# Optimization experiments

Hardware: AMD Instinct MI355X
Metric: run time of the kernel (lower is better)

Reference implementation:

```python
import jax, jax.numpy as jnp
import numpy as np

N_NODES = 50000
N_EDGES = 1600000
IN_CH, HID_CH, OUT_CH = 384, 128, 64


def gcn_conv(x, W, b, src, dst, num_nodes):
    """PyG GCNConv: add self-loops, symmetric deg^-1/2 normalization,
    linear transform, scatter-add aggregation, bias."""
    loop = jnp.arange(num_nodes, dtype=src.dtype)
    src2 = jnp.concatenate([src, loop])  # [E+N]
    dst2 = jnp.concatenate([dst, loop])
    deg = jax.ops.segment_sum(jnp.ones_like(dst2, dtype=x.dtype), dst2,
                              num_segments=num_nodes)
    dinv = jnp.where(deg > 0, jax.lax.rsqrt(deg), 0.0)
    norm = dinv[src2] * dinv[dst2]  # [E+N]
    h = x @ W  # [N, out]
    msg = h[src2] * norm[:, None]  # gather + scale
    out = jax.ops.segment_sum(msg, dst2, num_segments=num_nodes)
    return out + b


def setup_inputs() -> dict:
    key = jax.random.key(0)
    k1, k2, k3, k4 = jax.random.split(key, 4)
    x = jax.random.normal(k1, (N_NODES, IN_CH), dtype=jnp.float32)
    edge_index = jax.random.randint(k2, (2, N_EDGES), 0, N_NODES, dtype=jnp.int64)
    W1 = jax.random.normal(k3, (IN_CH, HID_CH), dtype=jnp.float32) / np.sqrt(IN_CH)
    b1 = jnp.zeros((HID_CH,), dtype=jnp.float32)
    W2 = jax.random.normal(k4, (HID_CH, OUT_CH), dtype=jnp.float32) / np.sqrt(HID_CH)
    b2 = jnp.zeros((OUT_CH,), dtype=jnp.float32)
    return {"x": x, "edge_index": edge_index, "W1": W1, "b1": b1, "W2": W2, "b2": b2}


def reference(x, edge_index, W1, b1, W2, b2):
    src, dst = edge_index[0], edge_index[1]
    h = gcn_conv(x, W1, b1, src, dst, N_NODES)
    h = jax.nn.relu(h)
    out = gcn_conv(h, W2, b2, src, dst, N_NODES)
    return out
```

## Files before the change

kernel.cpp:

```cpp
#include <hip/hip_runtime.h>

constexpr int NN  = 50000;
constexpr int NE  = 1600000;
constexpr int CIN = 384;
constexpr int CH  = 128;
constexpr int CO  = 64;

constexpr int NB = (NN + 255) / 256;
constexpr int BUCKET_CAP = 16384;
constexpr int SCAT_EPB     = 4096;
constexpr int SCAT_BLOCKS  = (NE + SCAT_EPB - 1) / SCAT_EPB;
constexpr int G1_TILES     = (NN + 127) / 128;
constexpr int G2_TILES     = (NN + 127) / 128;

typedef __attribute__((ext_vector_type(8))) short short8;
typedef __attribute__((ext_vector_type(4))) float f32x4;


__device__ inline unsigned short f2bf(float f) {
    union { float f; unsigned int u; } v; v.f = f;
    unsigned int u = v.u + 0x7FFFu + ((v.u >> 16) & 1u);
    return (unsigned short)(u >> 16);
}
__device__ inline float bf2f(unsigned short h) { return __uint_as_float((unsigned int)h << 16); }
__device__ inline float bflo(unsigned int u) { return __uint_as_float(u << 16); }
__device__ inline float bfhi(unsigned int u) { return __uint_as_float(u & 0xFFFF0000u); }


__global__ __launch_bounds__(256) void wprep(const float* __restrict__ W1, const float* __restrict__ W2,
                                             unsigned short* __restrict__ W1t_hi, unsigned short* __restrict__ W1t_lo,
                                             unsigned short* __restrict__ W2t_hi, unsigned short* __restrict__ W2t_lo,
                                             int* __restrict__ bucket_cursor) {
    int i = blockIdx.x * 256 + threadIdx.x;
    if (blockIdx.x == 0 && threadIdx.x < NB)
        bucket_cursor[threadIdx.x] = threadIdx.x * BUCKET_CAP;
    if (i < CIN * CH) {
        int k = i / CH, c = i % CH;
        float v = W1[i];
        unsigned short h = f2bf(v);
        W1t_hi[c * CIN + k] = h;
        W1t_lo[c * CIN + k] = f2bf(v - bf2f(h));
    } else if (i < CIN * CH + CH * CO) {
        int j = i - CIN * CH;
        int k = j / CO, c = j % CO;
        float v = W2[j];
        unsigned short h = f2bf(v);
        W2t_hi[c * CH + k] = h;
        W2t_lo[c * CH + k] = f2bf(v - bf2f(h));
    }
}


__global__ __launch_bounds__(256) void fused_gemm1_scatter(const int* __restrict__ src,
                                                           const int* __restrict__ dst,
                                                           int* __restrict__ bucket_cursor,
                                                           unsigned int* __restrict__ pairs,
                                                           const float* __restrict__ X,
                                                           const unsigned short* __restrict__ Wt_hi,
                                                           const unsigned short* __restrict__ Wt_lo,
                                                           unsigned short* __restrict__ Hb) {
    __shared__ unsigned short xs_hi[128][40];
    __shared__ unsigned short xs_lo[128][40];
    __shared__ unsigned short ws_hi[128][40];
    __shared__ unsigned short ws_lo[128][40];
    __shared__ int hist[NB];
    __shared__ int base_s[NB];

    int tid = threadIdx.x;
    if (blockIdx.x < SCAT_BLOCKS) {
        int e0 = blockIdx.x * SCAT_EPB;
        for (int i = tid; i < NB; i += 256) hist[i] = 0;
        __syncthreads();
        int key[16];
        unsigned int pay[16];
        #pragma unroll
        for (int k = 0; k < 16; ++k) {
            int e = e0 + k * 256 + tid;
            if (e < NE) {
                int s = src[e], d = dst[e];
                int b = d >> 8;
                int pos = atomicAdd(&hist[b], 1);
                key[k] = b | (pos << 8);
                pay[k] = (unsigned int)s | ((unsigned int)(d & 255) << 16);
            } else {
                key[k] = -1;
            }
        }
        __syncthreads();
        for (int i = tid; i < NB; i += 256)
            base_s[i] = hist[i] ? atomicAdd(&bucket_cursor[i], hist[i]) : 0;
        __syncthreads();
        #pragma unroll
        for (int k = 0; k < 16; ++k) {
            if (key[k] >= 0) {
                int b = key[k] & 255, pos = key[k] >> 8;
                pairs[base_s[b] + pos] = pay[k];
            }
        }
        return;
    }

    int wid = tid >> 6, lane = tid & 63;
    int row0 = (blockIdx.x - SCAT_BLOCKS) * 128;
    f32x4 acc[2][8] = {};

    int xrow = tid >> 1, xc = (tid & 1) * 16;
    int grow = row0 + xrow;
    int wcol = tid >> 2, wko = (tid & 3) * 8;

    float xf[16];
    short8 pwh0, pwl0, pwh1, pwl1;

    auto loadX = [&](int k0) {
        if (grow < NN) {
            const float4* p = reinterpret_cast<const float4*>(X + (size_t)grow * CIN + k0 + xc);
            float4 v0 = p[0], v1 = p[1], v2 = p[2], v3 = p[3];
            xf[0]=v0.x; xf[1]=v0.y; xf[2]=v0.z; xf[3]=v0.w;
            xf[4]=v1.x; xf[5]=v1.y; xf[6]=v1.z; xf[7]=v1.w;
            xf[8]=v2.x; xf[9]=v2.y; xf[10]=v2.z; xf[11]=v2.w;
            xf[12]=v3.x; xf[13]=v3.y; xf[14]=v3.z; xf[15]=v3.w;
        } else {
            #pragma unroll
            for (int i = 0; i < 16; ++i) xf[i] = 0.f;
        }
    };
    auto loadW = [&](int k0) {
        pwh0 = *reinterpret_cast<const short8*>(Wt_hi + (size_t)wcol * CIN + k0 + wko);
        pwl0 = *reinterpret_cast<const short8*>(Wt_lo + (size_t)wcol * CIN + k0 + wko);
        pwh1 = *reinterpret_cast<const short8*>(Wt_hi + (size_t)(wcol + 64) * CIN + k0 + wko);
        pwl1 = *reinterpret_cast<const short8*>(Wt_lo + (size_t)(wcol + 64) * CIN + k0 + wko);
    };

    loadX(0); loadW(0);
    for (int k0 = 0; k0 < CIN; k0 += 32) {
        {
            short8 vh0, vh1, vl0, vl1;
            #pragma unroll
            for (int i = 0; i < 8; ++i) {
                unsigned short h = f2bf(xf[i]);
                vh0[i] = (short)h; vl0[i] = (short)f2bf(xf[i] - bf2f(h));
            }
            #pragma unroll
            for (int i = 0; i < 8; ++i) {
                unsigned short h = f2bf(xf[8 + i]);
                vh1[i] = (short)h; vl1[i] = (short)f2bf(xf[8 + i] - bf2f(h));
            }
            *reinterpret_cast<short8*>(&xs_hi[xrow][xc])     = vh0;
            *reinterpret_cast<short8*>(&xs_hi[xrow][xc + 8]) = vh1;
            *reinterpret_cast<short8*>(&xs_lo[xrow][xc])     = vl0;
            *reinterpret_cast<short8*>(&xs_lo[xrow][xc + 8]) = vl1;
            *reinterpret_cast<short8*>(&ws_hi[wcol][wko])      = pwh0;
            *reinterpret_cast<short8*>(&ws_lo[wcol][wko])      = pwl0;
            *reinterpret_cast<short8*>(&ws_hi[wcol + 64][wko]) = pwh1;
            *reinterpret_cast<short8*>(&ws_lo[wcol + 64][wko]) = pwl1;
        }
        __syncthreads();
        if (k0 + 32 < CIN) { loadX(k0 + 32); loadW(k0 + 32); }
        int r = lane & 15, ko = (lane >> 4) * 8;
        short8 a_hi[2], a_lo[2];
        #pragma unroll
        for (int rt = 0; rt < 2; ++rt) {
            a_hi[rt] = *reinterpret_cast<const short8*>(&xs_hi[wid * 32 + rt * 16 + r][ko]);
            a_lo[rt] = *reinterpret_cast<const short8*>(&xs_lo[wid * 32 + rt * 16 + r][ko]);
        }
        #pragma unroll
        for (int ct = 0; ct < 8; ++ct) {
            short8 b_hi = *reinterpret_cast<const short8*>(&ws_hi[ct * 16 + r][ko]);
            short8 b_lo = *reinterpret_cast<const short8*>(&ws_lo[ct * 16 + r][ko]);
            #pragma unroll
            for (int rt = 0; rt < 2; ++rt) {
                acc[rt][ct] = __builtin_amdgcn_mfma_f32_16x16x32_bf16(a_hi[rt], b_hi, acc[rt][ct], 0, 0, 0);
                acc[rt][ct] = __builtin_amdgcn_mfma_f32_16x16x32_bf16(a_hi[rt], b_lo, acc[rt][ct], 0, 0, 0);
                acc[rt][ct] = __builtin_amdgcn_mfma_f32_16x16x32_bf16(a_lo[rt], b_hi, acc[rt][ct], 0, 0, 0);
            }
        }
        __syncthreads();
    }
    int cl = lane & 15, rg = lane >> 4;
    #pragma unroll
    for (int rt = 0; rt < 2; ++rt) {
        #pragma unroll
        for (int j = 0; j < 4; ++j) {
            int row = row0 + wid * 32 + rt * 16 + rg * 4 + j;
            if (row < NN) {
                unsigned short* hp = Hb + (size_t)row * CH + cl;
                #pragma unroll
                for (int ct = 0; ct < 8; ++ct)
                    hp[ct * 16] = f2bf(acc[rt][ct][j]);
            }
        }
    }
}


__global__ __launch_bounds__(256) void bucket_scan(const int* __restrict__ bucket_cursor,
                                                   int* __restrict__ bucket_start) {
    __shared__ int tmp[256];
    int t = threadIdx.x;
    int v = (t < NB) ? (bucket_cursor[t] - t * BUCKET_CAP) : 0;
    tmp[t] = v;
    __syncthreads();
    for (int off = 1; off < 256; off <<= 1) {
        int add = (t >= off) ? tmp[t - off] : 0;
        __syncthreads();
        tmp[t] += add;
        __syncthreads();
    }
    if (t < NB) bucket_start[t] = tmp[t] - v;
    if (t == NB - 1) bucket_start[NB] = tmp[t];
}


__global__ __launch_bounds__(1024) void bucket_sort(const unsigned int* __restrict__ pairs,
                                                    const int* __restrict__ bucket_cursor,
                                                    const int* __restrict__ bucket_start,
                                                    int* __restrict__ row_start,
                                                    float* __restrict__ dinv,
                                                    unsigned short* __restrict__ csr_src) {
    __shared__ int cnt[256];
    __shared__ int pref[256];
    __shared__ int cur[256];
    int b = blockIdx.x, t = threadIdx.x;
    int p0 = b * BUCKET_CAP;
    int ne = bucket_cursor[b] - p0;
    int out0 = bucket_start[b];
    if (t < 256) cnt[t] = 0;
    __syncthreads();
    for (int i = t; i < ne; i += 1024)
        atomicAdd(&cnt[(pairs[p0 + i] >> 16) & 255], 1);
    __syncthreads();
    if (t < 256) pref[t] = cnt[t];
    __syncthreads();
    for (int off = 1; off < 256; off <<= 1) {
        int add = (t < 256 && t >= off) ? pref[t - off] : 0;
        __syncthreads();
        if (t < 256) pref[t] += add;
        __syncthreads();
    }
    if (t < 256) {
        int n = (b << 8) + t;
        if (n < NN) {
            int rs = out0 + pref[t] - cnt[t];
            row_start[n] = rs;
            cur[t] = rs;
            dinv[n] = rsqrtf((float)(cnt[t] + 1));
        }
    }
    if (b == NB - 1 && t == 0) row_start[NN] = NE;
    __syncthreads();
    for (int i = t; i < ne; i += 1024) {
        unsigned int p = pairs[p0 + i];
        int pos = atomicAdd(&cur[(p >> 16) & 255], 1);
        csr_src[pos] = (unsigned short)(p & 0xFFFF);
    }
}


__global__ __launch_bounds__(256) void gemm2_kernel(const float* __restrict__ X,
                                                    const unsigned short* __restrict__ Wt_hi,
                                                    const unsigned short* __restrict__ Wt_lo,
                                                    unsigned short* __restrict__ Hb) {
    __shared__ unsigned short xs_hi[128][40];
    __shared__ unsigned short xs_lo[128][40];
    __shared__ unsigned short ws_hi[64][40];
    __shared__ unsigned short ws_lo[64][40];

    int tid = threadIdx.x;
    int wid = tid >> 6, lane = tid & 63;
    int row0 = blockIdx.x * 128;
    f32x4 acc[2][4] = {};

    for (int k0 = 0; k0 < CH; k0 += 32) {
        {
            int row = tid >> 1, c = (tid & 1) * 16;
            int grow = row0 + row;
            float f[16];
            if (grow < NN) {
                const float4* p = reinterpret_cast<const float4*>(X + (size_t)grow * CH + k0 + c);
                float4 v0 = p[0], v1 = p[1], v2 = p[2], v3 = p[3];
                f[0]=v0.x; f[1]=v0.y; f[2]=v0.z; f[3]=v0.w;
                f[4]=v1.x; f[5]=v1.y; f[6]=v1.z; f[7]=v1.w;
                f[8]=v2.x; f[9]=v2.y; f[10]=v2.z; f[11]=v2.w;
                f[12]=v3.x; f[13]=v3.y; f[14]=v3.z; f[15]=v3.w;
            } else {
                #pragma unroll
                for (int i = 0; i < 16; ++i) f[i] = 0.f;
            }
            short8 vh0, vh1, vl0, vl1;
            #pragma unroll
            for (int i = 0; i < 8; ++i) {
                unsigned short h = f2bf(f[i]);
                vh0[i] = (short)h; vl0[i] = (short)f2bf(f[i] - bf2f(h));
            }
            #pragma unroll
            for (int i = 0; i < 8; ++i) {
                unsigned short h = f2bf(f[8 + i]);
                vh1[i] = (short)h; vl1[i] = (short)f2bf(f[8 + i] - bf2f(h));
            }
            *reinterpret_cast<short8*>(&xs_hi[row][c])     = vh0;
            *reinterpret_cast<short8*>(&xs_hi[row][c + 8]) = vh1;
            *reinterpret_cast<short8*>(&xs_lo[row][c])     = vl0;
            *reinterpret_cast<short8*>(&xs_lo[row][c + 8]) = vl1;
        }
        if (tid < 256) {
            int col = tid >> 2, ko = (tid & 3) * 8;
            *reinterpret_cast<short8*>(&ws_hi[col][ko]) =
                *reinterpret_cast<const short8*>(Wt_hi + (size_t)col * CH + k0 + ko);
            *reinterpret_cast<short8*>(&ws_lo[col][ko]) =
                *reinterpret_cast<const short8*>(Wt_lo + (size_t)col * CH + k0 + ko);
        }
        __syncthreads();
        int r = lane & 15, ko = (lane >> 4) * 8;
        short8 a_hi[2], a_lo[2];
        #pragma unroll
        for (int rt = 0; rt < 2; ++rt) {
            a_hi[rt] = *reinterpret_cast<const short8*>(&xs_hi[wid * 32 + rt * 16 + r][ko]);
            a_lo[rt] = *reinterpret_cast<const short8*>(&xs_lo[wid * 32 + rt * 16 + r][ko]);
        }
        #pragma unroll
        for (int ct = 0; ct < 4; ++ct) {
            short8 b_hi = *reinterpret_cast<const short8*>(&ws_hi[ct * 16 + r][ko]);
            short8 b_lo = *reinterpret_cast<const short8*>(&ws_lo[ct * 16 + r][ko]);
            #pragma unroll
            for (int rt = 0; rt < 2; ++rt) {
                acc[rt][ct] = __builtin_amdgcn_mfma_f32_16x16x32_bf16(a_hi[rt], b_hi, acc[rt][ct], 0, 0, 0);
                acc[rt][ct] = __builtin_amdgcn_mfma_f32_16x16x32_bf16(a_hi[rt], b_lo, acc[rt][ct], 0, 0, 0);
                acc[rt][ct] = __builtin_amdgcn_mfma_f32_16x16x32_bf16(a_lo[rt], b_hi, acc[rt][ct], 0, 0, 0);
            }
        }
        __syncthreads();
    }
    int cl = lane & 15, rg = lane >> 4;
    #pragma unroll
    for (int rt = 0; rt < 2; ++rt) {
        #pragma unroll
        for (int j = 0; j < 4; ++j) {
            int row = row0 + wid * 32 + rt * 16 + rg * 4 + j;
            if (row < NN) {
                unsigned short* hp = Hb + (size_t)row * CO + cl;
                #pragma unroll
                for (int ct = 0; ct < 4; ++ct)
                    hp[ct * 16] = f2bf(acc[rt][ct][j]);
            }
        }
    }
}


__global__ __launch_bounds__(64) void agg1_kernel(const unsigned int* __restrict__ H,
                                                  const int* __restrict__ row_start,
                                                  const unsigned short* __restrict__ csr_src,
                                                  const float* __restrict__ dinv,
                                                  const float* __restrict__ bias,
                                                  float* __restrict__ OUT) {
    int n = blockIdx.x;
    int l = threadIdx.x;
    float dn = dinv[n];
    unsigned int us = H[n * 64 + l];
    float a0 = dn * bflo(us), a1 = dn * bfhi(us);
    float b0 = 0.f, b1 = 0.f, c0 = 0.f, c1 = 0.f, d0 = 0.f, d1 = 0.f;
    float e0a = 0.f, e1a = 0.f, f0 = 0.f, f1 = 0.f, g0 = 0.f, g1v = 0.f, h0 = 0.f, h1 = 0.f;
    int e0 = row_start[n], e1 = row_start[n + 1];
    for (int base = e0; base < e1; base += 64) {
        int m = min(64, e1 - base);
        int sv = csr_src[base + min(l, m - 1)];
        float wv = (l < m) ? dinv[sv] : 0.f;
        int j = 0;
        for (; j + 8 <= m; j += 8) {
            int s0 = __shfl(sv, j),     s1 = __shfl(sv, j + 1);
            int s2 = __shfl(sv, j + 2), s3 = __shfl(sv, j + 3);
            int s4 = __shfl(sv, j + 4), s5 = __shfl(sv, j + 5);
            int s6 = __shfl(sv, j + 6), s7 = __shfl(sv, j + 7);
            float w0 = __shfl(wv, j),     w1 = __shfl(wv, j + 1);
            float w2 = __shfl(wv, j + 2), w3 = __shfl(wv, j + 3);
            float w4 = __shfl(wv, j + 4), w5 = __shfl(wv, j + 5);
            float w6 = __shfl(wv, j + 6), w7 = __shfl(wv, j + 7);
            unsigned int u0 = H[s0 * 64 + l];
            unsigned int u1 = H[s1 * 64 + l];
            unsigned int u2 = H[s2 * 64 + l];
            unsigned int u3 = H[s3 * 64 + l];
            unsigned int u4 = H[s4 * 64 + l];
            unsigned int u5 = H[s5 * 64 + l];
            unsigned int u6 = H[s6 * 64 + l];
            unsigned int u7 = H[s7 * 64 + l];
            a0  = fmaf(w0, bflo(u0), a0);  a1  = fmaf(w0, bfhi(u0), a1);
            b0  = fmaf(w1, bflo(u1), b0);  b1  = fmaf(w1, bfhi(u1), b1);
            c0  = fmaf(w2, bflo(u2), c0);  c1  = fmaf(w2, bfhi(u2), c1);
            d0  = fmaf(w3, bflo(u3), d0);  d1  = fmaf(w3, bfhi(u3), d1);
            e0a = fmaf(w4, bflo(u4), e0a); e1a = fmaf(w4, bfhi(u4), e1a);
            f0  = fmaf(w5, bflo(u5), f0);  f1  = fmaf(w5, bfhi(u5), f1);
            g0  = fmaf(w6, bflo(u6), g0);  g1v = fmaf(w6, bfhi(u6), g1v);
            h0  = fmaf(w7, bflo(u7), h0);  h1  = fmaf(w7, bfhi(u7), h1);
        }
        for (; j < m; ++j) {
            int s0 = __shfl(sv, j);
            float w0 = __shfl(wv, j);
            unsigned int u0 = H[s0 * 64 + l];
            a0 = fmaf(w0, bflo(u0), a0); a1 = fmaf(w0, bfhi(u0), a1);
        }
    }
    float s0 = ((a0 + b0) + (c0 + d0)) + ((e0a + f0) + (g0 + h0));
    float s1 = ((a1 + b1) + (c1 + d1)) + ((e1a + f1) + (g1v + h1));
    float2 bv = reinterpret_cast<const float2*>(bias)[l];
    float o0 = fmaf(dn, s0, bv.x);
    float o1 = fmaf(dn, s1, bv.y);
    reinterpret_cast<float2*>(OUT)[n * 64 + l] = make_float2(fmaxf(o0, 0.f), fmaxf(o1, 0.f));
}

__global__ __launch_bounds__(64) void agg2_kernel(const unsigned int* __restrict__ H,
                                                  const int* __restrict__ row_start,
                                                  const unsigned short* __restrict__ csr_src,
                                                  const float* __restrict__ dinv,
                                                  const float* __restrict__ bias,
                                                  float* __restrict__ OUT) {
    int n = blockIdx.x;
    int l = threadIdx.x;
    int half = l >> 5;
    int c = l & 31;
    float dn = dinv[n];
    unsigned int us = H[n * 32 + c];
    float a0 = half ? 0.f : dn * bflo(us);
    float a1 = half ? 0.f : dn * bfhi(us);
    float b0 = 0.f, b1 = 0.f, c0 = 0.f, c1 = 0.f, d0 = 0.f, d1 = 0.f;
    int e0 = row_start[n], e1 = row_start[n + 1];
    for (int base = e0; base < e1; base += 64) {
        int m = min(64, e1 - base);
        int sv = csr_src[base + min(l, m - 1)];
        float wv = (l < m) ? dinv[sv] : 0.f;
        int j = 0;
        for (; j + 8 <= m; j += 8) {
            int jj0 = j + half, jj1 = j + 2 + half, jj2 = j + 4 + half, jj3 = j + 6 + half;
            int s0 = __shfl(sv, jj0), s1 = __shfl(sv, jj1);
            int s2 = __shfl(sv, jj2), s3 = __shfl(sv, jj3);
            float w0 = __shfl(wv, jj0), w1 = __shfl(wv, jj1);
            float w2 = __shfl(wv, jj2), w3 = __shfl(wv, jj3);
            unsigned int u0 = H[s0 * 32 + c];
            unsigned int u1 = H[s1 * 32 + c];
            unsigned int u2 = H[s2 * 32 + c];
            unsigned int u3 = H[s3 * 32 + c];
            a0 = fmaf(w0, bflo(u0), a0); a1 = fmaf(w0, bfhi(u0), a1);
            b0 = fmaf(w1, bflo(u1), b0); b1 = fmaf(w1, bfhi(u1), b1);
            c0 = fmaf(w2, bflo(u2), c0); c1 = fmaf(w2, bfhi(u2), c1);
            d0 = fmaf(w3, bflo(u3), d0); d1 = fmaf(w3, bfhi(u3), d1);
        }
        for (; j < m; j += 2) {
            int jj = j + half;
            int s = __shfl(sv, min(jj, m - 1));
            float w = __shfl(wv, jj);
            unsigned int u = H[s * 32 + c];
            a0 = fmaf(w, bflo(u), a0);
            a1 = fmaf(w, bfhi(u), a1);
        }
    }
    a0 = (a0 + b0) + (c0 + d0);
    a1 = (a1 + b1) + (c1 + d1);
    a0 += __shfl_xor(a0, 32);
    a1 += __shfl_xor(a1, 32);
    if (l < 32) {
        float2 bv = reinterpret_cast<const float2*>(bias)[c];
        float o0 = fmaf(dn, a0, bv.x);
        float o1 = fmaf(dn, a1, bv.y);
        reinterpret_cast<float2*>(OUT)[n * 32 + c] = make_float2(o0, o1);
    }
}


extern "C" void kernel_launch(void* const* d_in, const int* in_sizes, int n_in,
                              void* d_out, int out_size, void* d_ws, size_t ws_size,
                              hipStream_t stream) {
    const float* x  = (const float*)d_in[0];
    const int*   ei = (const int*)d_in[1];
    const float* W1 = (const float*)d_in[2];
    const float* b1 = (const float*)d_in[3];
    const float* W2 = (const float*)d_in[4];
    const float* b2 = (const float*)d_in[5];
    const int* srcI = ei;
    const int* dstI = ei + NE;
    float* out = (float*)d_out;

    char* ws = (char*)d_ws;
    size_t off = 0;
    auto take = [&](size_t bytes) {
        char* p = ws + off;
        off = (off + bytes + 255) & ~(size_t)255;
        return p;
    };
    int*            row_start     = (int*)take((size_t)(NN + 1) * 4);
    int*            bucket_cursor = (int*)take((size_t)NB * 4);
    int*            bucket_start  = (int*)take((size_t)(NB + 1) * 4);
    float*          dinv          = (float*)take((size_t)NN * 4);
    unsigned short* W1t_hi        = (unsigned short*)take((size_t)CH * CIN * 2);
    unsigned short* W1t_lo        = (unsigned short*)take((size_t)CH * CIN * 2);
    unsigned short* W2t_hi        = (unsigned short*)take((size_t)CO * CH * 2);
    unsigned short* W2t_lo        = (unsigned short*)take((size_t)CO * CH * 2);
    unsigned short* csr_src       = (unsigned short*)take((size_t)NE * 2);
    unsigned short* h1b           = (unsigned short*)take((size_t)NN * CH * 2);
    float*          g1            = (float*)take((size_t)NN * CH * 4);
    unsigned short* h2b           = (unsigned short*)take((size_t)NN * CO * 2);
    unsigned int*   pairs         = (unsigned int*)g1;

    wprep<<<(CIN * CH + CH * CO + 255) / 256, 256, 0, stream>>>(W1, W2, W1t_hi, W1t_lo,
                                                                W2t_hi, W2t_lo, bucket_cursor);
    fused_gemm1_scatter<<<SCAT_BLOCKS + G1_TILES, 256, 0, stream>>>(srcI, dstI, bucket_cursor,
                                                                    pairs, x, W1t_hi, W1t_lo, h1b);
    bucket_scan<<<1, 256, 0, stream>>>(bucket_cursor, bucket_start);
    bucket_sort<<<NB, 1024, 0, stream>>>(pairs, bucket_cursor, bucket_start,
                                         row_start, dinv, csr_src);

    agg1_kernel<<<NN, 64, 0, stream>>>((const unsigned int*)h1b, row_start, csr_src, dinv, b1, g1);
    gemm2_kernel<<<G2_TILES, 256, 0, stream>>>(g1, W2t_hi, W2t_lo, h2b);
    agg2_kernel<<<NN, 64, 0, stream>>>((const unsigned int*)h2b, row_start, csr_src, dinv, b2, out);
}
```

Measured before the change: 153.1 us.

## Fuse layer-2 GEMM into layer-1 aggregation and interleave scatter/GEMM1 blocks

The separate gemm2 MFMA kernel is removed. Each agg1 block now applies ReLU, then multiplies its 128-wide node row by W2 with a wavefront-shuffle GEMV in fp32, writing bf16 H2 directly. This avoids writing and rereading the fp32 g1 intermediate and drops a kernel launch, at the cost of 64x128 scalar W2 loads per node (served from cache). The fused scatter/GEMM1 launch also alternates scatter and GEMM blocks by parity instead of running all scatter blocks first, and pairs gets its own buffer.

```diff
diff --git a/kernel.cpp b/kernel.cpp
--- a/kernel.cpp
+++ b/kernel.cpp
@@ -11,7 +11,7 @@
 constexpr int SCAT_EPB     = 4096;
 constexpr int SCAT_BLOCKS  = (NE + SCAT_EPB - 1) / SCAT_EPB;
 constexpr int G1_TILES     = (NN + 127) / 128;
-constexpr int G2_TILES     = (NN + 127) / 128;
+static_assert(SCAT_BLOCKS == G1_TILES, "interleave assumes equal counts");
 
 typedef __attribute__((ext_vector_type(8))) short short8;
 typedef __attribute__((ext_vector_type(4))) float f32x4;
@@ -27,9 +27,9 @@
 __device__ inline float bfhi(unsigned int u) { return __uint_as_float(u & 0xFFFF0000u); }
 
 
-__global__ __launch_bounds__(256) void wprep(const float* __restrict__ W1, const float* __restrict__ W2,
-                                             unsigned short* __restrict__ W1t_hi, unsigned short* __restrict__ W1t_lo,
-                                             unsigned short* __restrict__ W2t_hi, unsigned short* __restrict__ W2t_lo,
+__global__ __launch_bounds__(256) void wprep(const float* __restrict__ W1,
+                                             unsigned short* __restrict__ W1t_hi,
+                                             unsigned short* __restrict__ W1t_lo,
                                              int* __restrict__ bucket_cursor) {
     int i = blockIdx.x * 256 + threadIdx.x;
     if (blockIdx.x == 0 && threadIdx.x < NB)
@@ -40,13 +40,6 @@
         unsigned short h = f2bf(v);
         W1t_hi[c * CIN + k] = h;
         W1t_lo[c * CIN + k] = f2bf(v - bf2f(h));
-    } else if (i < CIN * CH + CH * CO) {
-        int j = i - CIN * CH;
-        int k = j / CO, c = j % CO;
-        float v = W2[j];
-        unsigned short h = f2bf(v);
-        W2t_hi[c * CH + k] = h;
-        W2t_lo[c * CH + k] = f2bf(v - bf2f(h));
     }
 }
 
@@ -67,8 +60,9 @@
     __shared__ int base_s[NB];
 
     int tid = threadIdx.x;
-    if (blockIdx.x < SCAT_BLOCKS) {
-        int e0 = blockIdx.x * SCAT_EPB;
+    int sub = blockIdx.x >> 1;
+    if ((blockIdx.x & 1) == 0) {
+        int e0 = sub * SCAT_EPB;
         for (int i = tid; i < NB; i += 256) hist[i] = 0;
         __syncthreads();
         int key[16];
@@ -101,7 +95,7 @@
     }
 
     int wid = tid >> 6, lane = tid & 63;
-    int row0 = (blockIdx.x - SCAT_BLOCKS) * 128;
+    int row0 = sub * 128;
     f32x4 acc[2][8] = {};
 
     int xrow = tid >> 1, xc = (tid & 1) * 16;
@@ -256,103 +250,13 @@
 }
 
 
-__global__ __launch_bounds__(256) void gemm2_kernel(const float* __restrict__ X,
-                                                    const unsigned short* __restrict__ Wt_hi,
-                                                    const unsigned short* __restrict__ Wt_lo,
-                                                    unsigned short* __restrict__ Hb) {
-    __shared__ unsigned short xs_hi[128][40];
-    __shared__ unsigned short xs_lo[128][40];
-    __shared__ unsigned short ws_hi[64][40];
-    __shared__ unsigned short ws_lo[64][40];
-
-    int tid = threadIdx.x;
-    int wid = tid >> 6, lane = tid & 63;
-    int row0 = blockIdx.x * 128;
-    f32x4 acc[2][4] = {};
-
-    for (int k0 = 0; k0 < CH; k0 += 32) {
-        {
-            int row = tid >> 1, c = (tid & 1) * 16;
-            int grow = row0 + row;
-            float f[16];
-            if (grow < NN) {
-                const float4* p = reinterpret_cast<const float4*>(X + (size_t)grow * CH + k0 + c);
-                float4 v0 = p[0], v1 = p[1], v2 = p[2], v3 = p[3];
-                f[0]=v0.x; f[1]=v0.y; f[2]=v0.z; f[3]=v0.w;
-                f[4]=v1.x; f[5]=v1.y; f[6]=v1.z; f[7]=v1.w;
-                f[8]=v2.x; f[9]=v2.y; f[10]=v2.z; f[11]=v2.w;
-                f[12]=v3.x; f[13]=v3.y; f[14]=v3.z; f[15]=v3.w;
-            } else {
-                #pragma unroll
-                for (int i = 0; i < 16; ++i) f[i] = 0.f;
-            }
-            short8 vh0, vh1, vl0, vl1;
-            #pragma unroll
-            for (int i = 0; i < 8; ++i) {
-                unsigned short h = f2bf(f[i]);
-                vh0[i] = (short)h; vl0[i] = (short)f2bf(f[i] - bf2f(h));
-            }
-            #pragma unroll
-            for (int i = 0; i < 8; ++i) {
-                unsigned short h = f2bf(f[8 + i]);
-                vh1[i] = (short)h; vl1[i] = (short)f2bf(f[8 + i] - bf2f(h));
-            }
-            *reinterpret_cast<short8*>(&xs_hi[row][c])     = vh0;
-            *reinterpret_cast<short8*>(&xs_hi[row][c + 8]) = vh1;
-            *reinterpret_cast<short8*>(&xs_lo[row][c])     = vl0;
-            *reinterpret_cast<short8*>(&xs_lo[row][c + 8]) = vl1;
-        }
-        if (tid < 256) {
-            int col = tid >> 2, ko = (tid & 3) * 8;
-            *reinterpret_cast<short8*>(&ws_hi[col][ko]) =
-                *reinterpret_cast<const short8*>(Wt_hi + (size_t)col * CH + k0 + ko);
-            *reinterpret_cast<short8*>(&ws_lo[col][ko]) =
-                *reinterpret_cast<const short8*>(Wt_lo + (size_t)col * CH + k0 + ko);
-        }
-        __syncthreads();
-        int r = lane & 15, ko = (lane >> 4) * 8;
-        short8 a_hi[2], a_lo[2];
-        #pragma unroll
-        for (int rt = 0; rt < 2; ++rt) {
-            a_hi[rt] = *reinterpret_cast<const short8*>(&xs_hi[wid * 32 + rt * 16 + r][ko]);
-            a_lo[rt] = *reinterpret_cast<const short8*>(&xs_lo[wid * 32 + rt * 16 + r][ko]);
-        }
-        #pragma unroll
-        for (int ct = 0; ct < 4; ++ct) {
-            short8 b_hi = *reinterpret_cast<const short8*>(&ws_hi[ct * 16 + r][ko]);
-            short8 b_lo = *reinterpret_cast<const short8*>(&ws_lo[ct * 16 + r][ko]);
-            #pragma unroll
-            for (int rt = 0; rt < 2; ++rt) {
-                acc[rt][ct] = __builtin_amdgcn_mfma_f32_16x16x32_bf16(a_hi[rt], b_hi, acc[rt][ct], 0, 0, 0);
-                acc[rt][ct] = __builtin_amdgcn_mfma_f32_16x16x32_bf16(a_hi[rt], b_lo, acc[rt][ct], 0, 0, 0);
-                acc[rt][ct] = __builtin_amdgcn_mfma_f32_16x16x32_bf16(a_lo[rt], b_hi, acc[rt][ct], 0, 0, 0);
-            }
-        }
-        __syncthreads();
-    }
-    int cl = lane & 15, rg = lane >> 4;
-    #pragma unroll
-    for (int rt = 0; rt < 2; ++rt) {
-        #pragma unroll
-        for (int j = 0; j < 4; ++j) {
-            int row = row0 + wid * 32 + rt * 16 + rg * 4 + j;
-            if (row < NN) {
-                unsigned short* hp = Hb + (size_t)row * CO + cl;
-                #pragma unroll
-                for (int ct = 0; ct < 4; ++ct)
-                    hp[ct * 16] = f2bf(acc[rt][ct][j]);
-            }
-        }
-    }
-}
-
-
-__global__ __launch_bounds__(64) void agg1_kernel(const unsigned int* __restrict__ H,
-                                                  const int* __restrict__ row_start,
-                                                  const unsigned short* __restrict__ csr_src,
-                                                  const float* __restrict__ dinv,
-                                                  const float* __restrict__ bias,
-                                                  float* __restrict__ OUT) {
+__global__ __launch_bounds__(64) void agg1_gemv_kernel(const unsigned int* __restrict__ H,
+                                                       const int* __restrict__ row_start,
+                                                       const unsigned short* __restrict__ csr_src,
+                                                       const float* __restrict__ dinv,
+                                                       const float* __restrict__ bias,
+                                                       const float* __restrict__ W2,
+                                                       unsigned short* __restrict__ H2b) {
     int n = blockIdx.x;
     int l = threadIdx.x;
     float dn = dinv[n];
@@ -402,10 +306,20 @@
     float s0 = ((a0 + b0) + (c0 + d0)) + ((e0a + f0) + (g0 + h0));
     float s1 = ((a1 + b1) + (c1 + d1)) + ((e1a + f1) + (g1v + h1));
     float2 bv = reinterpret_cast<const float2*>(bias)[l];
-    float o0 = fmaf(dn, s0, bv.x);
-    float o1 = fmaf(dn, s1, bv.y);
-    reinterpret_cast<float2*>(OUT)[n * 64 + l] = make_float2(fmaxf(o0, 0.f), fmaxf(o1, 0.f));
-}
+    float o0 = fmaxf(fmaf(dn, s0, bv.x), 0.f);
+    float o1 = fmaxf(fmaf(dn, s1, bv.y), 0.f);
+
+    float hA = 0.f, hB = 0.f;
+    #pragma unroll 4
+    for (int sl = 0; sl < 64; sl += 2) {
+        float ga0 = __shfl(o0, sl),     ga1 = __shfl(o1, sl);
+        float gb0 = __shfl(o0, sl + 1), gb1 = __shfl(o1, sl + 1);
+        hA = fmaf(ga0, W2[(2 * sl) * 64 + l],     fmaf(ga1, W2[(2 * sl + 1) * 64 + l], hA));
+        hB = fmaf(gb0, W2[(2 * sl + 2) * 64 + l], fmaf(gb1, W2[(2 * sl + 3) * 64 + l], hB));
+    }
+    H2b[(size_t)n * 64 + l] = f2bf(hA + hB);
+}
+
 
 __global__ __launch_bounds__(64) void agg2_kernel(const unsigned int* __restrict__ H,
                                                   const int* __restrict__ row_start,
@@ -491,23 +405,19 @@
     float*          dinv          = (float*)take((size_t)NN * 4);
     unsigned short* W1t_hi        = (unsigned short*)take((size_t)CH * CIN * 2);
     unsigned short* W1t_lo        = (unsigned short*)take((size_t)CH * CIN * 2);
-    unsigned short* W2t_hi        = (unsigned short*)take((size_t)CO * CH * 2);
-    unsigned short* W2t_lo        = (unsigned short*)take((size_t)CO * CH * 2);
     unsigned short* csr_src       = (unsigned short*)take((size_t)NE * 2);
     unsigned short* h1b           = (unsigned short*)take((size_t)NN * CH * 2);
-    float*          g1            = (float*)take((size_t)NN * CH * 4);
     unsigned short* h2b           = (unsigned short*)take((size_t)NN * CO * 2);
-    unsigned int*   pairs         = (unsigned int*)g1;
-
-    wprep<<<(CIN * CH + CH * CO + 255) / 256, 256, 0, stream>>>(W1, W2, W1t_hi, W1t_lo,
-                                                                W2t_hi, W2t_lo, bucket_cursor);
+    unsigned int*   pairs         = (unsigned int*)take((size_t)NB * BUCKET_CAP * 4);
+
+    wprep<<<(CIN * CH + 255) / 256, 256, 0, stream>>>(W1, W1t_hi, W1t_lo, bucket_cursor);
     fused_gemm1_scatter<<<SCAT_BLOCKS + G1_TILES, 256, 0, stream>>>(srcI, dstI, bucket_cursor,
                                                                     pairs, x, W1t_hi, W1t_lo, h1b);
     bucket_scan<<<1, 256, 0, stream>>>(bucket_cursor, bucket_start);
     bucket_sort<<<NB, 1024, 0, stream>>>(pairs, bucket_cursor, bucket_start,
                                          row_start, dinv, csr_src);
 
-    agg1_kernel<<<NN, 64, 0, stream>>>((const unsigned int*)h1b, row_start, csr_src, dinv, b1, g1);
-    gemm2_kernel<<<G2_TILES, 256, 0, stream>>>(g1, W2t_hi, W2t_lo, h2b);
+    agg1_gemv_kernel<<<NN, 64, 0, stream>>>((const unsigned int*)h1b, row_start, csr_src,
+                                            dinv, b1, W2, h2b);
     agg2_kernel<<<NN, 64, 0, stream>>>((const unsigned int*)h2b, row_start, csr_src, dinv, b2, out);
 }
```

After: 201.5 us. 1.32x slower.
